# Optimization experiments

Hardware: AMD Instinct MI355X
Metric: run time of the kernel (lower is better)

Reference implementation:

```python
import jax, jax.numpy as jnp
import numpy as np

RES = 32          # resolution (32, 32) -> N = 1024 tokens
HEADS = 16
EMB = 1024
BATCH = 8
N = RES * RES


def _bias_idxs(res):
    # relative-offset index table, [N, N] with values in [0, res*res)
    coords = np.stack(np.meshgrid(np.arange(res), np.arange(res), indexing='ij'), -1).reshape(-1, 2)
    d = np.abs(coords[:, None, :] - coords[None, :, :])  # [N, N, 2]
    return jnp.asarray(d[..., 0] * res + d[..., 1], dtype=jnp.int64)


def setup_inputs() -> dict:
    key = jax.random.key(0)
    k1, k2, k3, k4, k5 = jax.random.split(key, 5)
    x = jax.random.normal(k1, (BATCH, N, EMB), dtype=jnp.float32)
    w_qkv = jax.random.normal(k2, (3 * EMB, EMB), dtype=jnp.float32) * 0.02
    biases = jax.random.normal(k3, (HEADS, RES * RES), dtype=jnp.float32) * 0.02
    bias_idxs = _bias_idxs(RES)
    w_out = jax.random.normal(k4, (EMB, EMB), dtype=jnp.float32) * 0.02
    b_out = jax.random.normal(k5, (EMB,), dtype=jnp.float32) * 0.02
    return {"x": x, "w_qkv": w_qkv, "biases": biases,
            "bias_idxs": bias_idxs, "w_out": w_out, "b_out": b_out}


def reference(x, w_qkv, biases, bias_idxs, w_out, b_out):
    b, n, e = x.shape
    h = HEADS
    d = e // h
    scale = d ** -0.5
    # to_qkv: Linear(e, 3e, bias=False); torch Linear computes x @ W.T
    qkv = x @ w_qkv.T                                   # [b, n, 3e]
    q, k, v = jnp.split(qkv, 3, axis=-1)
    def to_heads(t):
        return t.reshape(b, n, h, d).transpose(0, 2, 1, 3)  # b h n d
    q, k, v = to_heads(q), to_heads(k), to_heads(v)
    scores = jnp.einsum('bhid,bhjd->bhij', q, k) * scale    # [b, h, n, n]
    scores = scores + biases[:, bias_idxs]                  # gather -> [h, n, n], broadcast over b
    attn = jax.nn.softmax(scores, axis=-1)
    out = jnp.einsum('bhij,bhjd->bhid', attn, v)            # [b, h, n, d]
    out = out.transpose(0, 2, 1, 3).reshape(b, n, e)        # b n (h d)
    # to_out: Linear(e, e) with bias (dropout = identity at inference)
    return out @ w_out.T + b_out
```

## Files before the change

kernel.cpp:

```cpp
#include <hip/hip_runtime.h>
#include <stdint.h>


#define LOG2E 1.4426950408889634f
#define QSCL 0.18033688011112042f

typedef __attribute__((ext_vector_type(8))) short short8;
typedef __attribute__((ext_vector_type(4))) short short4v;
typedef __attribute__((ext_vector_type(4))) float floatx4;
typedef __attribute__((ext_vector_type(2))) unsigned int uint2v;
typedef __attribute__((ext_vector_type(4))) unsigned int uint4v;

__device__ __forceinline__ short f2bf(float f) {
  uint32_t u = __builtin_bit_cast(uint32_t, f);
  u = (u + 0x7FFFu + ((u >> 16) & 1u)) >> 16;
  return (short)(uint16_t)u;
}
__device__ __forceinline__ float bf2f(short s) {
  uint32_t u = ((uint32_t)(uint16_t)s) << 16;
  return __builtin_bit_cast(float, u);
}
__device__ __forceinline__ float fast_exp2(float x) {
#if __has_builtin(__builtin_amdgcn_exp2f)
  return __builtin_amdgcn_exp2f(x);
#else
  return exp2f(x);
#endif
}

__device__ __forceinline__ void gload_lds16(const short* g, short* l) {
  __builtin_amdgcn_global_load_lds(
      (const __attribute__((address_space(1))) void*)g,
      (__attribute__((address_space(3))) void*)l, 16, 0, 0);
}

__global__ void prep(const float* __restrict__ x, const float* __restrict__ wqkv,
                     const float* __restrict__ wout, const float* __restrict__ biases,
                     short* __restrict__ xb, short* __restrict__ wqkvb,
                     short* __restrict__ woutb, short* __restrict__ biast) {
  int blk = blockIdx.x, tid = threadIdx.x;
  if (blk < 12288) {
    const float* src;
    short* dst;
    int i;
    if (blk < 8192) { src = x; dst = xb; i = blk * 256 + tid; }
    else if (blk < 11264) { src = wqkv; dst = wqkvb; i = (blk - 8192) * 256 + tid; }
    else { src = wout; dst = woutb; i = (blk - 11264) * 256 + tid; }
    float4 f = ((const float4*)src)[i];
    short4v o;
    o.x = f2bf(f.x); o.y = f2bf(f.y); o.z = f2bf(f.z); o.w = f2bf(f.w);
    ((short4v*)dst)[i] = o;
  } else {
    int tile = (blk - 12288) * 4 + (tid >> 6);
    int lane = tid & 63, qd = lane >> 4, col = lane & 15;
    int bp = tile & 1, ap = (tile >> 1) & 1, dra = (tile >> 2) & 31, h = tile >> 7;
    int ci = 16 * bp + col;
    short4v o;
#pragma unroll
    for (int r = 0; r < 4; r++) {
      int cj = 16 * ap + 4 * qd + r;
      int dc = cj - ci; if (dc < 0) dc = -dc;
      o[r] = f2bf(biases[h * 1024 + dra * 32 + dc] * LOG2E);
    }
    *(short4v*)&biast[(size_t)tile * 256 + lane * 4] = o;
  }
}

template <int MODE>
__global__ __launch_bounds__(256, 3) void gemm_bt(
    const short* __restrict__ A, const short* __restrict__ Bt,
    short* __restrict__ qo, short* __restrict__ ko, short* __restrict__ vto,
    const float* __restrict__ bvec, float* __restrict__ outf) {
  __shared__ __align__(16) short sA[128 * 64];
  __shared__ __align__(16) short sB[128 * 64];
  const int tid = threadIdx.x;
  const int w = tid >> 6, lane = tid & 63;
  const int wr = w >> 1, wc = w & 1;
  const int bm = blockIdx.y, bn = blockIdx.x;
  const int qd = lane >> 4, col = lane & 15;

  floatx4 acc[4][4] = {};
  const int rowA0 = bm * 128, rowB0 = bn * 128;
  const int ciw = w * 256;

  for (int kk = 0; kk < 1024; kk += 64) {
    __syncthreads();
#pragma unroll
    for (int n = 0; n < 4; n++) {
      int ci = ciw + n * 64 + lane;
      int r = ci >> 3, c = (ci & 7) ^ (r & 7);
      gload_lds16(A + (size_t)(rowA0 + r) * 1024 + kk + c * 8, &sA[ci * 8]);
    }
#pragma unroll
    for (int n = 0; n < 4; n++) {
      int ci = ciw + n * 64 + lane;
      int r = ci >> 3, c = (ci & 7) ^ (r & 7);
      gload_lds16(Bt + (size_t)(rowB0 + r) * 1024 + kk + c * 8, &sB[ci * 8]);
    }
    __syncthreads();

#pragma unroll
    for (int ks = 0; ks < 2; ks++) {
      const int ch = qd + ks * 4;
      short8 af[4], bff[4];
#pragma unroll
      for (int rt = 0; rt < 4; rt++) {
        int r = wr * 64 + rt * 16 + col;
        af[rt] = *(const short8*)&sA[r * 64 + ((ch ^ (r & 7)) << 3)];
      }
#pragma unroll
      for (int ct = 0; ct < 4; ct++) {
        int r = wc * 64 + ct * 16 + col;
        bff[ct] = *(const short8*)&sB[r * 64 + ((ch ^ (r & 7)) << 3)];
      }
#pragma unroll
      for (int rt = 0; rt < 4; rt++)
#pragma unroll
        for (int ct = 0; ct < 4; ct++)
          acc[rt][ct] = __builtin_amdgcn_mfma_f32_16x16x32_bf16(af[rt], bff[ct], acc[rt][ct], 0, 0, 0);
    }
  }

  if (MODE == 0) {
    if (bn >= 16) {
#pragma unroll
      for (int rt = 0; rt < 4; rt++) {
#pragma unroll
        for (int ct = 0; ct < 4; ct++) {
          int Cg = bn * 128 + wc * 64 + ct * 16 + col;
          int e = Cg & 1023, h = e >> 6, dd = e & 63;
          short4v pv;
#pragma unroll
          for (int r = 0; r < 4; r++) pv[r] = f2bf(acc[rt][ct][r]);
          int R0 = bm * 128 + wr * 64 + rt * 16 + qd * 4;
          int b = R0 >> 10, n0 = R0 & 1023;
          int bh = b * 16 + h;
          *(short4v*)&vto[((size_t)bh * 64 + dd) * 1024 + n0] = pv;
        }
      }
    } else {
#pragma unroll
      for (int rt = 0; rt < 4; rt++) {
#pragma unroll
        for (int ct = 0; ct < 4; ct++) {
          int Cg = bn * 128 + wc * 64 + ct * 16 + col;
          int which = Cg >> 10, e = Cg & 1023, h = e >> 6, dd = e & 63;
#pragma unroll
          for (int r = 0; r < 4; r++) {
            int R = bm * 128 + wr * 64 + rt * 16 + qd * 4 + r;
            int b = R >> 10, n = R & 1023;
            int bh = b * 16 + h;
            float av = acc[rt][ct][r];
            if (which == 0) av *= QSCL;
            short v = f2bf(av);
            if (which == 0)
              qo[((size_t)bh * 1024 + n) * 64 + dd] = v;
            else
              ko[((size_t)bh * 1024 + n) * 64 + dd] = v;
          }
        }
      }
    }
  } else {
#pragma unroll
    for (int rt = 0; rt < 4; rt++)
#pragma unroll
      for (int ct = 0; ct < 4; ct++) {
        int Cg = bn * 128 + wc * 64 + ct * 16 + col;
        float bo = bvec[Cg];
#pragma unroll
        for (int r = 0; r < 4; r++) {
          int R = bm * 128 + wr * 64 + rt * 16 + qd * 4 + r;
          outf[(size_t)R * 1024 + Cg] = acc[rt][ct][r] + bo;
        }
      }
  }
}

__global__ __launch_bounds__(256, 3) void attn_fused(
    const short* __restrict__ q, const short* __restrict__ k,
    const short* __restrict__ vt, const short* __restrict__ biast,
    short* __restrict__ ao) {
  __shared__ __align__(16) short smem[20480];
  short* sQ = smem;
  short* sK = smem + 4096;
  short* sVt = smem + 12288;
  const int tid = threadIdx.x, w = tid >> 6, lane = tid & 63;
  const int id = blockIdx.x;
  const int sid = (id & 7) * 256 + (id >> 3);
  const int bh = sid >> 4, qt = sid & 15;
  const int h = bh & 15;
  const int qd = lane >> 4, col = lane & 15;
  const short* qb = q + (size_t)bh * 65536;
  const short* kb = k + (size_t)bh * 65536;
  const short* vb = vt + (size_t)bh * 65536;
  const int ciw = w * 256;

#pragma unroll
  for (int n = 0; n < 2; n++) {
    int ci = w * 128 + n * 64 + lane;
    int r = ci >> 3, c = (ci & 7) ^ (r & 7);
    gload_lds16(qb + (size_t)(qt * 64 + r) * 64 + c * 8, &sQ[ci * 8]);
  }

  floatx4 oacc[4][4] = {};
  float rs[4] = {0.f, 0.f, 0.f, 0.f};

  for (int js = 0; js < 8; js++) {
#pragma unroll
    for (int n = 0; n < 4; n++) {
      int ci = ciw + n * 64 + lane;
      int r = ci >> 3, c = (ci & 7) ^ (r & 7);
      gload_lds16(kb + (size_t)(js * 128 + r) * 64 + c * 8, &sK[ci * 8]);
    }
#pragma unroll
    for (int n = 0; n < 4; n++) {
      int ci = ciw + n * 64 + lane;
      int r = ci >> 4, c = (ci & 15) ^ (r & 15);
      gload_lds16(vb + (size_t)r * 1024 + js * 128 + c * 8, &sVt[ci * 8]);
    }
    __syncthreads();

    uint32_t pw[4][4];
#pragma unroll
    for (int rt = 0; rt < 2; rt++) {
      const int a = js * 8 + w * 2 + rt;
      const int ar = a >> 1, ap = a & 1;
      short4v bfrag[4];
#pragma unroll
      for (int ct = 0; ct < 4; ct++) {
        int b = qt * 4 + ct;
        int dra = ar - (b >> 1); if (dra < 0) dra = -dra;
        int tile = ((h * 32 + dra) * 2 + ap) * 2 + (b & 1);
        bfrag[ct] = *(const short4v*)&biast[(size_t)tile * 256 + lane * 4];
      }
      const int r = w * 32 + rt * 16 + col;
      floatx4 sacc[4];
#pragma unroll
      for (int ct = 0; ct < 4; ct++) {
        sacc[ct][0] = bf2f(bfrag[ct][0]);
        sacc[ct][1] = bf2f(bfrag[ct][1]);
        sacc[ct][2] = bf2f(bfrag[ct][2]);
        sacc[ct][3] = bf2f(bfrag[ct][3]);
      }
      __builtin_amdgcn_s_setprio(1);
#pragma unroll
      for (int ks = 0; ks < 2; ks++) {
        const int ch = qd + ks * 4;
        short8 ak = *(const short8*)&sK[r * 64 + ((ch ^ (r & 7)) << 3)];
        short8 bqf[4];
#pragma unroll
        for (int ct = 0; ct < 4; ct++) {
          int r2 = ct * 16 + col;
          bqf[ct] = *(const short8*)&sQ[r2 * 64 + ((ch ^ (r2 & 7)) << 3)];
        }
#pragma unroll
        for (int ct = 0; ct < 4; ct++)
          sacc[ct] = __builtin_amdgcn_mfma_f32_16x16x32_bf16(ak, bqf[ct], sacc[ct], 0, 0, 0);
      }
      __builtin_amdgcn_s_setprio(0);
#pragma unroll
      for (int ct = 0; ct < 4; ct++) {
        float e0 = fast_exp2(sacc[ct][0]);
        float e1 = fast_exp2(sacc[ct][1]);
        float e2 = fast_exp2(sacc[ct][2]);
        float e3 = fast_exp2(sacc[ct][3]);
        rs[ct] += (e0 + e1) + (e2 + e3);
        uint32_t u0 = __builtin_bit_cast(uint32_t, e0) + 0x8000u;
        uint32_t u1 = __builtin_bit_cast(uint32_t, e1) + 0x8000u;
        uint32_t u2 = __builtin_bit_cast(uint32_t, e2) + 0x8000u;
        uint32_t u3 = __builtin_bit_cast(uint32_t, e3) + 0x8000u;
        pw[ct][2 * rt + 0] = __builtin_amdgcn_perm(u1, u0, 0x07060302u);
        pw[ct][2 * rt + 1] = __builtin_amdgcn_perm(u3, u2, 0x07060302u);
      }
    }

    short8 pa[4], bv[4];
#pragma unroll
    for (int ct = 0; ct < 4; ct++)
      pa[ct] = __builtin_bit_cast(short8, (uint4v){pw[ct][0], pw[ct][1], pw[ct][2], pw[ct][3]});
    const int jc0 = 4 * w + (qd >> 1), off = 4 * (qd & 1);
#pragma unroll
    for (int ct = 0; ct < 4; ct++) {
      int d = ct * 16 + col;
      short4v lo4 = *(const short4v*)&sVt[d * 128 + ((jc0 ^ (d & 15)) << 3) + off];
      short4v hi4 = *(const short4v*)&sVt[d * 128 + (((jc0 + 2) ^ (d & 15)) << 3) + off];
      bv[ct] = __builtin_shufflevector(lo4, hi4, 0, 1, 2, 3, 4, 5, 6, 7);
    }
    __builtin_amdgcn_s_setprio(1);
#pragma unroll
    for (int ci2 = 0; ci2 < 4; ci2++)
#pragma unroll
      for (int cd = 0; cd < 4; cd++)
        oacc[ci2][cd] = __builtin_amdgcn_mfma_f32_16x16x32_bf16(pa[ci2], bv[cd], oacc[ci2][cd], 0, 0, 0);
    __builtin_amdgcn_s_setprio(0);
    __syncthreads();
  }

  float* fs = (float*)smem;
#pragma unroll
  for (int ct = 0; ct < 4; ct++)
    fs[(w * 4 + qd) * 64 + 16 * ct + col] = rs[ct];
  __syncthreads();
  {
    float tot = 0.f;
#pragma unroll
    for (int kk = 0; kk < 16; kk++) tot += fs[kk * 64 + lane];
    fs[1024 + lane] = 1.0f / tot;
  }
  __syncthreads();
  float myinv[8];
  if (w < 2) {
#pragma unroll
    for (int t2 = 0; t2 < 2; t2++)
#pragma unroll
      for (int r = 0; r < 4; r++)
        myinv[t2 * 4 + r] = fs[1024 + (w * 2 + t2) * 16 + 4 * qd + r];
  }
  __syncthreads();
  if (w >= 2) {
    float* ob = fs + (w - 2) * 4096;
#pragma unroll
    for (int ci2 = 0; ci2 < 4; ci2++)
#pragma unroll
      for (int cd = 0; cd < 4; cd++)
        *(floatx4*)&ob[((ci2 * 4 + cd) * 64 + lane) * 4] = oacc[ci2][cd];
  }
  __syncthreads();
  if (w < 2) {
    float* ob = fs + w * 4096;
#pragma unroll
    for (int ci2 = 0; ci2 < 4; ci2++)
#pragma unroll
      for (int cd = 0; cd < 4; cd++)
        oacc[ci2][cd] += *(const floatx4*)&ob[((ci2 * 4 + cd) * 64 + lane) * 4];
  }
  __syncthreads();
  if (w == 1) {
#pragma unroll
    for (int t2 = 0; t2 < 2; t2++)
#pragma unroll
      for (int cd = 0; cd < 4; cd++)
        *(floatx4*)&fs[((t2 * 4 + cd) * 64 + lane) * 4] = oacc[t2][cd];
  }
  if (w == 0) {
#pragma unroll
    for (int t2 = 0; t2 < 2; t2++)
#pragma unroll
      for (int cd = 0; cd < 4; cd++)
        *(floatx4*)&fs[2048 + ((t2 * 4 + cd) * 64 + lane) * 4] = oacc[2 + t2][cd];
  }
  __syncthreads();
  const int b = bh >> 4;
  if (w == 0) {
#pragma unroll
    for (int t2 = 0; t2 < 2; t2++) {
#pragma unroll
      for (int cd = 0; cd < 4; cd++) {
        floatx4 p = *(const floatx4*)&fs[((t2 * 4 + cd) * 64 + lane) * 4];
        floatx4 o = (t2 == 0 ? oacc[0][cd] : oacc[1][cd]);
        o += p;
#pragma unroll
        for (int r = 0; r < 4; r++) {
          int i = 16 * t2 + 4 * qd + r;
          int n = qt * 64 + i;
          int dd = cd * 16 + col;
          ao[(((size_t)b * 1024 + n) << 10) + h * 64 + dd] = f2bf(o[r] * myinv[t2 * 4 + r]);
        }
      }
    }
  } else if (w == 1) {
#pragma unroll
    for (int t2 = 0; t2 < 2; t2++) {
#pragma unroll
      for (int cd = 0; cd < 4; cd++) {
        floatx4 p = *(const floatx4*)&fs[2048 + ((t2 * 4 + cd) * 64 + lane) * 4];
        floatx4 o = (t2 == 0 ? oacc[2][cd] : oacc[3][cd]);
        o += p;
#pragma unroll
        for (int r = 0; r < 4; r++) {
          int i = 16 * (2 + t2) + 4 * qd + r;
          int n = qt * 64 + i;
          int dd = cd * 16 + col;
          ao[(((size_t)b * 1024 + n) << 10) + h * 64 + dd] = f2bf(o[r] * myinv[t2 * 4 + r]);
        }
      }
    }
  }
}

extern "C" void kernel_launch(void* const* d_in, const int* in_sizes, int n_in,
                              void* d_out, int out_size, void* d_ws, size_t ws_size,
                              hipStream_t stream) {
  const float* x = (const float*)d_in[0];
  const float* w_qkv = (const float*)d_in[1];
  const float* biases = (const float*)d_in[2];
  const float* w_out = (const float*)d_in[4];
  const float* b_out = (const float*)d_in[5];
  float* out = (float*)d_out;

  char* ws = (char*)d_ws;
  short* xb    = (short*)(ws + 0);
  short* wqkvb = (short*)(ws + 16777216);
  short* woutb = (short*)(ws + 23068672);
  short* qb    = (short*)(ws + 25165824);
  short* kb    = (short*)(ws + 41943040);
  short* vtb   = (short*)(ws + 58720256);
  short* aob   = (short*)(ws + 75497472);
  short* biast = (short*)(ws + 92274688);

  prep<<<13312, 256, 0, stream>>>(x, w_qkv, w_out, biases, xb, wqkvb, woutb, biast);
  gemm_bt<0><<<dim3(24, 64), 256, 0, stream>>>(xb, wqkvb, qb, kb, vtb, nullptr, nullptr);
  attn_fused<<<2048, 256, 0, stream>>>(qb, kb, vtb, biast, aob);
  gemm_bt<1><<<dim3(8, 64), 256, 0, stream>>>(aob, woutb, nullptr, nullptr, nullptr, b_out, out);
}
```

Baseline: 238.9 us.

## Split K tile into two 64-row halves to shrink LDS footprint

```diff
diff --git a/kernel.cpp b/kernel.cpp
--- a/kernel.cpp
+++ b/kernel.cpp
@@ -177,14 +177,68 @@
   }
 }
 
+#define QKT_PHASE(JSV, PARLIT)                                                 \
+  {                                                                            \
+    const int a_ = (JSV) * 4 + w;                                              \
+    const int ar_ = a_ >> 1, ap_ = a_ & 1;                                     \
+    short4v bfrag_[4];                                                         \
+    _Pragma("unroll")                                                          \
+    for (int ct = 0; ct < 4; ct++) {                                           \
+      int b_ = qt * 4 + ct;                                                    \
+      int dra_ = ar_ - (b_ >> 1); if (dra_ < 0) dra_ = -dra_;                  \
+      int tile_ = ((h * 32 + dra_) * 2 + ap_) * 2 + (b_ & 1);                  \
+      bfrag_[ct] = *(const short4v*)&biast[(size_t)tile_ * 256 + lane * 4];    \
+    }                                                                          \
+    const int r_ = w * 16 + col;                                               \
+    floatx4 sacc_[4];                                                          \
+    _Pragma("unroll")                                                          \
+    for (int ct = 0; ct < 4; ct++) {                                           \
+      sacc_[ct][0] = bf2f(bfrag_[ct][0]);                                      \
+      sacc_[ct][1] = bf2f(bfrag_[ct][1]);                                      \
+      sacc_[ct][2] = bf2f(bfrag_[ct][2]);                                      \
+      sacc_[ct][3] = bf2f(bfrag_[ct][3]);                                      \
+    }                                                                          \
+    __builtin_amdgcn_s_setprio(1);                                             \
+    _Pragma("unroll")                                                          \
+    for (int ks = 0; ks < 2; ks++) {                                           \
+      const int ch_ = qd + ks * 4;                                             \
+      short8 ak_ = *(const short8*)&sK[r_ * 64 + ((ch_ ^ (r_ & 7)) << 3)];     \
+      short8 bqf_[4];                                                          \
+      _Pragma("unroll")                                                        \
+      for (int ct = 0; ct < 4; ct++) {                                         \
+        int r2_ = ct * 16 + col;                                               \
+        bqf_[ct] = *(const short8*)&sQ[r2_ * 64 + ((ch_ ^ (r2_ & 7)) << 3)];   \
+      }                                                                        \
+      _Pragma("unroll")                                                        \
+      for (int ct = 0; ct < 4; ct++)                                           \
+        sacc_[ct] = __builtin_amdgcn_mfma_f32_16x16x32_bf16(ak_, bqf_[ct],     \
+                                                            sacc_[ct], 0, 0, 0); \
+    }                                                                          \
+    __builtin_amdgcn_s_setprio(0);                                             \
+    _Pragma("unroll")                                                          \
+    for (int ct = 0; ct < 4; ct++) {                                           \
+      float e0 = fast_exp2(sacc_[ct][0]);                                      \
+      float e1 = fast_exp2(sacc_[ct][1]);                                      \
+      float e2 = fast_exp2(sacc_[ct][2]);                                      \
+      float e3 = fast_exp2(sacc_[ct][3]);                                      \
+      rs[ct] += (e0 + e1) + (e2 + e3);                                         \
+      uint32_t u0 = __builtin_bit_cast(uint32_t, e0) + 0x8000u;                \
+      uint32_t u1 = __builtin_bit_cast(uint32_t, e1) + 0x8000u;                \
+      uint32_t u2 = __builtin_bit_cast(uint32_t, e2) + 0x8000u;                \
+      uint32_t u3 = __builtin_bit_cast(uint32_t, e3) + 0x8000u;                \
+      pw[ct][2 * (PARLIT) + 0] = __builtin_amdgcn_perm(u1, u0, 0x07060302u);   \
+      pw[ct][2 * (PARLIT) + 1] = __builtin_amdgcn_perm(u3, u2, 0x07060302u);   \
+    }                                                                          \
+  }
+
 __global__ __launch_bounds__(256, 3) void attn_fused(
     const short* __restrict__ q, const short* __restrict__ k,
     const short* __restrict__ vt, const short* __restrict__ biast,
     short* __restrict__ ao) {
-  __shared__ __align__(16) short smem[20480];
+  __shared__ __align__(16) short smem[16384];
   short* sQ = smem;
   short* sK = smem + 4096;
-  short* sVt = smem + 12288;
+  short* sVt = smem + 8192;
   const int tid = threadIdx.x, w = tid >> 6, lane = tid & 63;
   const int id = blockIdx.x;
   const int sid = (id & 7) * 256 + (id >> 3);
@@ -194,7 +248,6 @@
   const short* qb = q + (size_t)bh * 65536;
   const short* kb = k + (size_t)bh * 65536;
   const short* vb = vt + (size_t)bh * 65536;
-  const int ciw = w * 256;
 
 #pragma unroll
   for (int n = 0; n < 2; n++) {
@@ -206,85 +259,44 @@
   floatx4 oacc[4][4] = {};
   float rs[4] = {0.f, 0.f, 0.f, 0.f};
 
-  for (int js = 0; js < 8; js++) {
+  for (int jp = 0; jp < 8; jp++) {
+    uint32_t pw[4][4];
+
+#pragma unroll
+    for (int n = 0; n < 2; n++) {
+      int ci = w * 128 + n * 64 + lane;
+      int r = ci >> 3, c = (ci & 7) ^ (r & 7);
+      gload_lds16(kb + (size_t)(2 * jp * 64 + r) * 64 + c * 8, &sK[ci * 8]);
+    }
 #pragma unroll
     for (int n = 0; n < 4; n++) {
-      int ci = ciw + n * 64 + lane;
+      int ci = w * 256 + n * 64 + lane;
+      int r = ci >> 4, c = (ci & 15) ^ (r & 15);
+      gload_lds16(vb + (size_t)r * 1024 + jp * 128 + c * 8, &sVt[ci * 8]);
+    }
+    __syncthreads();
+    QKT_PHASE(2 * jp, 0)
+    __syncthreads();
+
+#pragma unroll
+    for (int n = 0; n < 2; n++) {
+      int ci = w * 128 + n * 64 + lane;
       int r = ci >> 3, c = (ci & 7) ^ (r & 7);
-      gload_lds16(kb + (size_t)(js * 128 + r) * 64 + c * 8, &sK[ci * 8]);
-    }
-#pragma unroll
-    for (int n = 0; n < 4; n++) {
-      int ci = ciw + n * 64 + lane;
-      int r = ci >> 4, c = (ci & 15) ^ (r & 15);
-      gload_lds16(vb + (size_t)r * 1024 + js * 128 + c * 8, &sVt[ci * 8]);
-    }
-    __syncthreads();
-
-    uint32_t pw[4][4];
-#pragma unroll
-    for (int rt = 0; rt < 2; rt++) {
-      const int a = js * 8 + w * 2 + rt;
-      const int ar = a >> 1, ap = a & 1;
-      short4v bfrag[4];
-#pragma unroll
-      for (int ct = 0; ct < 4; ct++) {
-        int b = qt * 4 + ct;
-        int dra = ar - (b >> 1); if (dra < 0) dra = -dra;
-        int tile = ((h * 32 + dra) * 2 + ap) * 2 + (b & 1);
-        bfrag[ct] = *(const short4v*)&biast[(size_t)tile * 256 + lane * 4];
-      }
-      const int r = w * 32 + rt * 16 + col;
-      floatx4 sacc[4];
-#pragma unroll
-      for (int ct = 0; ct < 4; ct++) {
-        sacc[ct][0] = bf2f(bfrag[ct][0]);
-        sacc[ct][1] = bf2f(bfrag[ct][1]);
-        sacc[ct][2] = bf2f(bfrag[ct][2]);
-        sacc[ct][3] = bf2f(bfrag[ct][3]);
-      }
-      __builtin_amdgcn_s_setprio(1);
-#pragma unroll
-      for (int ks = 0; ks < 2; ks++) {
-        const int ch = qd + ks * 4;
-        short8 ak = *(const short8*)&sK[r * 64 + ((ch ^ (r & 7)) << 3)];
-        short8 bqf[4];
-#pragma unroll
-        for (int ct = 0; ct < 4; ct++) {
-          int r2 = ct * 16 + col;
-          bqf[ct] = *(const short8*)&sQ[r2 * 64 + ((ch ^ (r2 & 7)) << 3)];
-        }
-#pragma unroll
-        for (int ct = 0; ct < 4; ct++)
-          sacc[ct] = __builtin_amdgcn_mfma_f32_16x16x32_bf16(ak, bqf[ct], sacc[ct], 0, 0, 0);
-      }
-      __builtin_amdgcn_s_setprio(0);
-#pragma unroll
-      for (int ct = 0; ct < 4; ct++) {
-        float e0 = fast_exp2(sacc[ct][0]);
-        float e1 = fast_exp2(sacc[ct][1]);
-        float e2 = fast_exp2(sacc[ct][2]);
-        float e3 = fast_exp2(sacc[ct][3]);
-        rs[ct] += (e0 + e1) + (e2 + e3);
-        uint32_t u0 = __builtin_bit_cast(uint32_t, e0) + 0x8000u;
-        uint32_t u1 = __builtin_bit_cast(uint32_t, e1) + 0x8000u;
-        uint32_t u2 = __builtin_bit_cast(uint32_t, e2) + 0x8000u;
-        uint32_t u3 = __builtin_bit_cast(uint32_t, e3) + 0x8000u;
-        pw[ct][2 * rt + 0] = __builtin_amdgcn_perm(u1, u0, 0x07060302u);
-        pw[ct][2 * rt + 1] = __builtin_amdgcn_perm(u3, u2, 0x07060302u);
-      }
-    }
+      gload_lds16(kb + (size_t)((2 * jp + 1) * 64 + r) * 64 + c * 8, &sK[ci * 8]);
+    }
+    __syncthreads();
+    QKT_PHASE(2 * jp + 1, 1)
 
     short8 pa[4], bv[4];
 #pragma unroll
     for (int ct = 0; ct < 4; ct++)
       pa[ct] = __builtin_bit_cast(short8, (uint4v){pw[ct][0], pw[ct][1], pw[ct][2], pw[ct][3]});
-    const int jc0 = 4 * w + (qd >> 1), off = 4 * (qd & 1);
+    const int jc0 = 2 * w + (qd >> 1), off = 4 * (qd & 1);
 #pragma unroll
     for (int ct = 0; ct < 4; ct++) {
       int d = ct * 16 + col;
       short4v lo4 = *(const short4v*)&sVt[d * 128 + ((jc0 ^ (d & 15)) << 3) + off];
-      short4v hi4 = *(const short4v*)&sVt[d * 128 + (((jc0 + 2) ^ (d & 15)) << 3) + off];
+      short4v hi4 = *(const short4v*)&sVt[d * 128 + (((jc0 + 8) ^ (d & 15)) << 3) + off];
       bv[ct] = __builtin_shufflevector(lo4, hi4, 0, 1, 2, 3, 4, 5, 6, 7);
     }
     __builtin_amdgcn_s_setprio(1);
```

Result: slower. 254.6 us (+6.6%).
